# Kernel tuning notes

Hardware: AMD Instinct MI355X
Metric: run time of the kernel (lower is better)

## Reference

```python
import jax, jax.numpy as jnp
import numpy as np

N = 50000
E = 800000
D_IN, D_HID = 64, 128
EPS = 0.0


def setup_inputs() -> dict:
    key = jax.random.key(0)
    k1, k2, k3, k4 = jax.random.split(key, 4)
    x = jax.random.normal(k1, (N, D_IN), dtype=jnp.float32)
    edge_index = jax.random.randint(k2, (2, E), 0, N, dtype=jnp.int32)
    W1 = jax.random.normal(k3, (D_IN, D_HID), dtype=jnp.float32) * (1.0 / np.sqrt(D_IN))
    b1 = jnp.zeros((D_HID,), dtype=jnp.float32)
    W2 = jax.random.normal(k4, (D_HID, D_IN), dtype=jnp.float32) * (1.0 / np.sqrt(D_HID))
    b2 = jnp.zeros((D_IN,), dtype=jnp.float32)
    return {"x": x, "edge_index": edge_index, "W1": W1, "b1": b1, "W2": W2, "b2": b2}


def reference(x, edge_index, W1, b1, W2, b2):
    src = edge_index[0]
    dst = edge_index[1]
    # gather source node features [E, d] and scatter-add into destination nodes [N, d]
    agg = jax.ops.segment_sum(x[src], dst, num_segments=N)
    h = agg + (1.0 + EPS) * x
    # GIN MLP: Linear -> ReLU -> Linear
    h = jax.nn.relu(h @ W1 + b1)
    return h @ W2 + b2
```

## Files before the change

### kernel.cpp

```cpp
#include <hip/hip_runtime.h>

#define N_NODES 50000
#define N_EDGES 800000
#define D_INF 64
#define D_HIDF 128

#define NBUCKET ((N_NODES + 63) / 64)
#define CHUNK 4096
#define NCHUNK ((N_EDGES + CHUNK - 1) / CHUNK)
#define CAP 4096

typedef __attribute__((ext_vector_type(8))) short bf16x8v;
typedef __attribute__((ext_vector_type(4))) float f32x4;

__device__ __forceinline__ ushort f2bf(float f) {
    unsigned int u = __builtin_bit_cast(unsigned int, f);
    u += 0x7FFF + ((u >> 16) & 1);
    return (ushort)(u >> 16);
}
__device__ __forceinline__ float bf2f(ushort u) {
    return __builtin_bit_cast(float, ((unsigned int)u) << 16);
}
__device__ __forceinline__ float bflo(unsigned int w) {
    return __builtin_bit_cast(float, w << 16);
}
__device__ __forceinline__ float bfhi(unsigned int w) {
    return __builtin_bit_cast(float, w & 0xFFFF0000u);
}


#define CVT_N (N_NODES * D_INF / 8)
#define PREP_N (D_INF * D_HIDF)

__global__ void prep_kernel(const float* __restrict__ x, ushort* __restrict__ xb,
                            const float* __restrict__ W1, const float* __restrict__ W2,
                            ushort* __restrict__ w1tb, ushort* __restrict__ w2tb,
                            int* __restrict__ gcursor) {
    int gid = blockIdx.x * blockDim.x + threadIdx.x;
    if (gid < CVT_N) {
        float4 a = reinterpret_cast<const float4*>(x)[gid * 2];
        float4 b = reinterpret_cast<const float4*>(x)[gid * 2 + 1];
        ushort o[8] = {f2bf(a.x), f2bf(a.y), f2bf(a.z), f2bf(a.w),
                       f2bf(b.x), f2bf(b.y), f2bf(b.z), f2bf(b.w)};
        *reinterpret_cast<ulonglong2*>(xb + gid * 8) = *reinterpret_cast<ulonglong2*>(o);
    } else if (gid < CVT_N + PREP_N) {
        int i = gid - CVT_N;
        int j = i >> 6, l = i & 63;
        w1tb[i] = f2bf(W1[l * D_HIDF + j]);
        int d = i >> 7, jj = i & 127;
        w2tb[i] = f2bf(W2[jj * D_INF + d]);
    } else if (gid < CVT_N + PREP_N + NBUCKET) {
        int b = gid - CVT_N - PREP_N;
        gcursor[b] = b * CAP;
    } else if (gid < CVT_N + PREP_N + NBUCKET + 8) {
        int i = gid - CVT_N - PREP_N - NBUCKET;
        ulonglong2 z;
        z.x = 0; z.y = 0;
        *reinterpret_cast<ulonglong2*>(xb + (size_t)N_NODES * D_INF + i * 8) = z;
    }
}


__global__ void __launch_bounds__(512) sortfill_kernel(const int* __restrict__ src,
                                                       const int* __restrict__ dst,
                                                       int* __restrict__ gcursor,
                                                       unsigned int* __restrict__ binned) {
    __shared__ int cnt[NBUCKET];
    __shared__ int off[NBUCKET];
    __shared__ int cur[NBUCKET];
    __shared__ int gbase[NBUCKET];
    __shared__ unsigned int buf[CHUNK];
    __shared__ int wsum[8];

    int t = threadIdx.x;
    int lane = t & 63;
    int wv = t >> 6;
    int base = blockIdx.x * CHUNK;
    int chunk_n = min(CHUNK, N_EDGES - base);

    for (int i = t; i < NBUCKET; i += 512) cnt[i] = 0;
    __syncthreads();

    unsigned int pkr[8];
    int bkt[8];
#pragma unroll
    for (int k = 0; k < 8; k++) {
        int e = base + k * 512 + t;
        bkt[k] = -1;
        pkr[k] = 0;
        if (e < N_EDGES) {
            int d = dst[e];
            int s = src[e];
            pkr[k] = ((unsigned int)d << 16) | (unsigned int)s;
            bkt[k] = d >> 6;
            atomicAdd(&cnt[bkt[k]], 1);
        }
    }
    __syncthreads();

    {
        int b0 = t * 2;
        int v0 = (b0 < NBUCKET) ? cnt[b0] : 0;
        int v1 = (b0 + 1 < NBUCKET) ? cnt[b0 + 1] : 0;
        int s = v0 + v1;
        int incl = s;
#pragma unroll
        for (int o = 1; o < 64; o <<= 1) {
            int u = __shfl_up(incl, o);
            if (lane >= o) incl += u;
        }
        if (lane == 63) wsum[wv] = incl;
        __syncthreads();
        if (t == 0) {
#pragma unroll
            for (int w = 1; w < 8; w++) wsum[w] += wsum[w - 1];
        }
        __syncthreads();
        int run = ((wv > 0) ? wsum[wv - 1] : 0) + (incl - s);
        if (b0 < NBUCKET) {
            off[b0] = run;
            cur[b0] = run;
            if (v0 > 0) gbase[b0] = atomicAdd(&gcursor[b0], v0);
        }
        run += v0;
        if (b0 + 1 < NBUCKET) {
            off[b0 + 1] = run;
            cur[b0 + 1] = run;
            if (v1 > 0) gbase[b0 + 1] = atomicAdd(&gcursor[b0 + 1], v1);
        }
    }
    __syncthreads();

#pragma unroll
    for (int k = 0; k < 8; k++) {
        if (bkt[k] >= 0) {
            int r = atomicAdd(&cur[bkt[k]], 1);
            buf[r] = pkr[k];
        }
    }
    __syncthreads();

#pragma unroll
    for (int k = 0; k < CHUNK / 512; k++) {
        int slot = k * 512 + t;
        if (slot < chunk_n) {
            unsigned int pk = buf[slot];
            int b = pk >> 22;
            int idx = gbase[b] + (slot - off[b]);
            if (idx < (b + 1) * CAP) binned[idx] = pk;
        }
    }
}


#define AT_LD 72
#define HT_LD 136

__global__ void __launch_bounds__(1024) mega_kernel(
    const ushort* __restrict__ xb, const unsigned int* __restrict__ binned,
    const int* __restrict__ gcursor,
    const ushort* __restrict__ w1tb, const float* __restrict__ b1v,
    const ushort* __restrict__ w2tb, const float* __restrict__ b2v,
    float* __restrict__ out)
{
    __shared__ unsigned int seg[CAP];
    __shared__ unsigned int sorted[CAP + 16];
    __shared__ __align__(16) ushort atile[64 * AT_LD];
    __shared__ __align__(16) ushort htile[64 * HT_LD];
    __shared__ int c64[64];
    __shared__ int rb[65];
    __shared__ int o64[64];

    int t = threadIdx.x;
    int lane = t & 63;
    int wv = t >> 6;
    int b = blockIdx.x;
    int beg = b * CAP;
    int cnt = min(gcursor[b] - beg, CAP);
    int nb = b * 64;
    int nvalid = min(64, N_NODES - nb);

    if (t < 64) c64[t] = 0;
    __syncthreads();

    for (int i = t; i < cnt; i += 1024) {
        unsigned int pk = binned[beg + i];
        seg[i] = pk;
        atomicAdd(&c64[(pk >> 16) & 63], 1);
    }
    __syncthreads();
    if (t < 64) {
        int v = c64[t];
        int incl = v;
#pragma unroll
        for (int off = 1; off < 64; off <<= 1) {
            int u = __shfl_up(incl, off);
            if (t >= off) incl += u;
        }
        rb[t] = incl - v;
        o64[t] = incl - v;
        if (t == 63) rb[64] = incl;
    }
    __syncthreads();
    for (int i = t; i < cnt; i += 1024) {
        unsigned int pk = seg[i];
        int pos = atomicAdd(&o64[(pk >> 16) & 63], 1);
        sorted[pos] = pk;
    }
    __syncthreads();

    int g4 = lane >> 4;
    int f4 = lane & 15;
#pragma unroll
    for (int k = 0; k < 4; k++) {
        int n = wv * 4 + k;
        float a0 = 0.f, a1 = 0.f, a2 = 0.f, a3 = 0.f;
        if (n < nvalid) {
            int e = rb[n];
            int end = rb[n + 1];
#pragma unroll 2
            for (; e < end; e += 16) {
                int i0 = e + 0 + g4;
                int i1 = e + 4 + g4;
                int i2 = e + 8 + g4;
                int i3 = e + 12 + g4;
                unsigned int pk0 = (i0 < end) ? sorted[i0] : (unsigned int)N_NODES;
                unsigned int pk1 = (i1 < end) ? sorted[i1] : (unsigned int)N_NODES;
                unsigned int pk2 = (i2 < end) ? sorted[i2] : (unsigned int)N_NODES;
                unsigned int pk3 = (i3 < end) ? sorted[i3] : (unsigned int)N_NODES;
                uint2 v0 = *reinterpret_cast<const uint2*>(
                    &xb[(size_t)(pk0 & 0xFFFFu) * D_INF + f4 * 4]);
                uint2 v1 = *reinterpret_cast<const uint2*>(
                    &xb[(size_t)(pk1 & 0xFFFFu) * D_INF + f4 * 4]);
                uint2 v2 = *reinterpret_cast<const uint2*>(
                    &xb[(size_t)(pk2 & 0xFFFFu) * D_INF + f4 * 4]);
                uint2 v3 = *reinterpret_cast<const uint2*>(
                    &xb[(size_t)(pk3 & 0xFFFFu) * D_INF + f4 * 4]);
                a0 += bflo(v0.x); a1 += bfhi(v0.x); a2 += bflo(v0.y); a3 += bfhi(v0.y);
                a0 += bflo(v1.x); a1 += bfhi(v1.x); a2 += bflo(v1.y); a3 += bfhi(v1.y);
                a0 += bflo(v2.x); a1 += bfhi(v2.x); a2 += bflo(v2.y); a3 += bfhi(v2.y);
                a0 += bflo(v3.x); a1 += bfhi(v3.x); a2 += bflo(v3.y); a3 += bfhi(v3.y);
            }
            a0 += __shfl_xor(a0, 16); a0 += __shfl_xor(a0, 32);
            a1 += __shfl_xor(a1, 16); a1 += __shfl_xor(a1, 32);
            a2 += __shfl_xor(a2, 16); a2 += __shfl_xor(a2, 32);
            a3 += __shfl_xor(a3, 16); a3 += __shfl_xor(a3, 32);
        }
        if (g4 == 0 && n < 64) {
            if (n < nvalid) {
                uint2 v = *reinterpret_cast<const uint2*>(
                    &xb[(size_t)(nb + n) * D_INF + f4 * 4]);
                a0 += bflo(v.x); a1 += bfhi(v.x);
                a2 += bflo(v.y); a3 += bfhi(v.y);
            }
            unsigned int w0 = (unsigned int)f2bf(a0) | ((unsigned int)f2bf(a1) << 16);
            unsigned int w1 = (unsigned int)f2bf(a2) | ((unsigned int)f2bf(a3) << 16);
            *reinterpret_cast<uint2*>(&atile[n * AT_LD + f4 * 4]) = make_uint2(w0, w1);
        }
    }
    __syncthreads();

    int q = lane >> 4;
    int m = lane & 15;
    int mt = wv & 3;
    int arow = mt * 16 + m;
    int hrow0 = mt * 16 + q * 4;

    bf16x8v a0v = *reinterpret_cast<const bf16x8v*>(&atile[arow * AT_LD + q * 8]);
    bf16x8v a1v = *reinterpret_cast<const bf16x8v*>(&atile[arow * AT_LD + 32 + q * 8]);
    int jt0 = (wv >> 2) * 2;
#pragma unroll
    for (int jj = 0; jj < 2; jj++) {
        int j = (jt0 + jj) * 16 + m;
        bf16x8v bf0 = *reinterpret_cast<const bf16x8v*>(w1tb + j * D_INF + q * 8);
        bf16x8v bf1 = *reinterpret_cast<const bf16x8v*>(w1tb + j * D_INF + 32 + q * 8);
        f32x4 acc = {0.f, 0.f, 0.f, 0.f};
        acc = __builtin_amdgcn_mfma_f32_16x16x32_bf16(a0v, bf0, acc, 0, 0, 0);
        acc = __builtin_amdgcn_mfma_f32_16x16x32_bf16(a1v, bf1, acc, 0, 0, 0);
        float bv = b1v[j];
#pragma unroll
        for (int r = 0; r < 4; r++) {
            float hv = fmaxf(acc[r] + bv, 0.f);
            htile[(hrow0 + r) * HT_LD + j] = f2bf(hv);
        }
    }
    __syncthreads();

    bf16x8v ha0 = *reinterpret_cast<const bf16x8v*>(&htile[arow * HT_LD + 0 * 32 + q * 8]);
    bf16x8v ha1 = *reinterpret_cast<const bf16x8v*>(&htile[arow * HT_LD + 1 * 32 + q * 8]);
    bf16x8v ha2 = *reinterpret_cast<const bf16x8v*>(&htile[arow * HT_LD + 2 * 32 + q * 8]);
    bf16x8v ha3 = *reinterpret_cast<const bf16x8v*>(&htile[arow * HT_LD + 3 * 32 + q * 8]);
    {
        int d = (wv >> 2) * 16 + m;
        bf16x8v bw0 = *reinterpret_cast<const bf16x8v*>(w2tb + d * D_HIDF + 0 * 32 + q * 8);
        bf16x8v bw1 = *reinterpret_cast<const bf16x8v*>(w2tb + d * D_HIDF + 1 * 32 + q * 8);
        bf16x8v bw2 = *reinterpret_cast<const bf16x8v*>(w2tb + d * D_HIDF + 2 * 32 + q * 8);
        bf16x8v bw3 = *reinterpret_cast<const bf16x8v*>(w2tb + d * D_HIDF + 3 * 32 + q * 8);
        f32x4 acc = {0.f, 0.f, 0.f, 0.f};
        acc = __builtin_amdgcn_mfma_f32_16x16x32_bf16(ha0, bw0, acc, 0, 0, 0);
        acc = __builtin_amdgcn_mfma_f32_16x16x32_bf16(ha1, bw1, acc, 0, 0, 0);
        acc = __builtin_amdgcn_mfma_f32_16x16x32_bf16(ha2, bw2, acc, 0, 0, 0);
        acc = __builtin_amdgcn_mfma_f32_16x16x32_bf16(ha3, bw3, acc, 0, 0, 0);
        float bv = b2v[d];
#pragma unroll
        for (int r = 0; r < 4; r++) {
            int node = nb + hrow0 + r;
            if (node < N_NODES) out[(size_t)node * D_INF + d] = acc[r] + bv;
        }
    }
}


#define W1_LD 72
#define W2_LD 136

__global__ void __launch_bounds__(256) mlp_mfma_kernel(
    const ushort* __restrict__ aggb, const ushort* __restrict__ w1tb,
    const float* __restrict__ b1v, const ushort* __restrict__ w2tb,
    const float* __restrict__ b2v, float* __restrict__ out)
{
    __shared__ __align__(16) ushort atile[64 * AT_LD];
    __shared__ __align__(16) ushort w1s[128 * W1_LD];
    __shared__ __align__(16) ushort w2s[64 * W2_LD];
    __shared__ __align__(16) ushort htile[64 * HT_LD];

    int tid = threadIdx.x;
    int lane = tid & 63;
    int wv = tid >> 6;
    int nb = blockIdx.x * 64;

#pragma unroll
    for (int c = 0; c < 2; c++) {
        int chunk = tid + c * 256;
        int row = chunk >> 3;
        int col = (chunk & 7) * 8;
        ulonglong2 v;
        v.x = 0; v.y = 0;
        if (nb + row < N_NODES)
            v = *reinterpret_cast<const ulonglong2*>(aggb + (size_t)(nb + row) * D_INF + col);
        *reinterpret_cast<ulonglong2*>(&atile[row * AT_LD + col]) = v;
    }
#pragma unroll
    for (int c = 0; c < 4; c++) {
        int chunk = tid + c * 256;
        int row = chunk >> 3;
        int col = (chunk & 7) * 8;
        *reinterpret_cast<ulonglong2*>(&w1s[row * W1_LD + col]) =
            *reinterpret_cast<const ulonglong2*>(w1tb + row * 64 + col);
    }
#pragma unroll
    for (int c = 0; c < 4; c++) {
        int chunk = tid + c * 256;
        int row = chunk >> 4;
        int col = (chunk & 15) * 8;
        *reinterpret_cast<ulonglong2*>(&w2s[row * W2_LD + col]) =
            *reinterpret_cast<const ulonglong2*>(w2tb + row * 128 + col);
    }
    __syncthreads();

    int q = lane >> 4;
    int m = lane & 15;
    int arow = wv * 16 + m;
    int hrow0 = wv * 16 + q * 4;

    bf16x8v a0 = *reinterpret_cast<const bf16x8v*>(&atile[arow * AT_LD + q * 8]);
    bf16x8v a1 = *reinterpret_cast<const bf16x8v*>(&atile[arow * AT_LD + 32 + q * 8]);
#pragma unroll
    for (int jt = 0; jt < 8; jt++) {
        int j = jt * 16 + m;
        bf16x8v bf0 = *reinterpret_cast<const bf16x8v*>(&w1s[j * W1_LD + q * 8]);
        bf16x8v bf1 = *reinterpret_cast<const bf16x8v*>(&w1s[j * W1_LD + 32 + q * 8]);
        f32x4 acc = {0.f, 0.f, 0.f, 0.f};
        acc = __builtin_amdgcn_mfma_f32_16x16x32_bf16(a0, bf0, acc, 0, 0, 0);
        acc = __builtin_amdgcn_mfma_f32_16x16x32_bf16(a1, bf1, acc, 0, 0, 0);
        float bv = b1v[j];
#pragma unroll
        for (int r = 0; r < 4; r++) {
            float hv = fmaxf(acc[r] + bv, 0.f);
            htile[(hrow0 + r) * HT_LD + j] = f2bf(hv);
        }
    }

    bf16x8v ha0 = *reinterpret_cast<const bf16x8v*>(&htile[arow * HT_LD + 0 * 32 + q * 8]);
    bf16x8v ha1 = *reinterpret_cast<const bf16x8v*>(&htile[arow * HT_LD + 1 * 32 + q * 8]);
    bf16x8v ha2 = *reinterpret_cast<const bf16x8v*>(&htile[arow * HT_LD + 2 * 32 + q * 8]);
    bf16x8v ha3 = *reinterpret_cast<const bf16x8v*>(&htile[arow * HT_LD + 3 * 32 + q * 8]);
#pragma unroll
    for (int dt = 0; dt < 4; dt++) {
        int d = dt * 16 + m;
        f32x4 acc = {0.f, 0.f, 0.f, 0.f};
        bf16x8v bw0 = *reinterpret_cast<const bf16x8v*>(&w2s[d * W2_LD + 0 * 32 + q * 8]);
        bf16x8v bw1 = *reinterpret_cast<const bf16x8v*>(&w2s[d * W2_LD + 1 * 32 + q * 8]);
        bf16x8v bw2 = *reinterpret_cast<const bf16x8v*>(&w2s[d * W2_LD + 2 * 32 + q * 8]);
        bf16x8v bw3 = *reinterpret_cast<const bf16x8v*>(&w2s[d * W2_LD + 3 * 32 + q * 8]);
        acc = __builtin_amdgcn_mfma_f32_16x16x32_bf16(ha0, bw0, acc, 0, 0, 0);
        acc = __builtin_amdgcn_mfma_f32_16x16x32_bf16(ha1, bw1, acc, 0, 0, 0);
        acc = __builtin_amdgcn_mfma_f32_16x16x32_bf16(ha2, bw2, acc, 0, 0, 0);
        acc = __builtin_amdgcn_mfma_f32_16x16x32_bf16(ha3, bw3, acc, 0, 0, 0);
        float bv = b2v[d];
#pragma unroll
        for (int r = 0; r < 4; r++) {
            int node = nb + hrow0 + r;
            if (node < N_NODES) out[(size_t)node * D_INF + d] = acc[r] + bv;
        }
    }
}

__global__ void init_agg_kernel(const float* __restrict__ x, float* __restrict__ agg) {
    int i = blockIdx.x * blockDim.x + threadIdx.x;
    int n4 = N_NODES * D_INF / 4;
    if (i < n4) {
        reinterpret_cast<float4*>(agg)[i] = reinterpret_cast<const float4*>(x)[i];
    }
}

__global__ void scatter_kernel(const float* __restrict__ x,
                               const int* __restrict__ src,
                               const int* __restrict__ dst,
                               float* __restrict__ agg) {
    int tid = blockIdx.x * blockDim.x + threadIdx.x;
    int e = tid >> 6;
    int d = tid & 63;
    if (e < N_EDGES) {
        atomicAdd(&agg[(size_t)dst[e] * D_INF + d], x[(size_t)src[e] * D_INF + d]);
    }
}

__global__ void cvt_agg_kernel(const float* __restrict__ agg32, ushort* __restrict__ aggb) {
    int i = blockIdx.x * blockDim.x + threadIdx.x;
    if (i < N_NODES * D_INF) aggb[i] = f2bf(agg32[i]);
}

__global__ void prep_weights_only_kernel(const float* __restrict__ W1,
                                         const float* __restrict__ W2,
                                         ushort* __restrict__ w1tb,
                                         ushort* __restrict__ w2tb) {
    int i = blockIdx.x * blockDim.x + threadIdx.x;
    if (i < D_INF * D_HIDF) {
        int j = i >> 6, l = i & 63;
        w1tb[i] = f2bf(W1[l * D_HIDF + j]);
        int d = i >> 7, jj = i & 127;
        w2tb[i] = f2bf(W2[jj * D_INF + d]);
    }
}


extern "C" void kernel_launch(void* const* d_in, const int* in_sizes, int n_in,
                              void* d_out, int out_size, void* d_ws, size_t ws_size,
                              hipStream_t stream) {
    const float* x   = (const float*)d_in[0];
    const int* edge  = (const int*)d_in[1];
    const float* W1  = (const float*)d_in[2];
    const float* b1  = (const float*)d_in[3];
    const float* W2  = (const float*)d_in[4];
    const float* b2  = (const float*)d_in[5];
    float* out       = (float*)d_out;

    const int* src = edge;
    const int* dst = edge + N_EDGES;

    ushort* w1tb   = (ushort*)d_ws;
    ushort* w2tb   = w1tb + D_INF * D_HIDF;
    ushort* xb     = w2tb + D_INF * D_HIDF;
    int* gcursor   = (int*)(xb + (size_t)(N_NODES + 1) * D_INF);
    unsigned int* binned = (unsigned int*)(gcursor + NBUCKET);
    float* agg32   = (float*)xb;
    ushort* aggb   = (ushort*)(binned + (size_t)NBUCKET * CAP);

    size_t needed_full = (uintptr_t)(binned + (size_t)NBUCKET * CAP) - (uintptr_t)d_ws;
    size_t needed_fb   = (uintptr_t)(aggb + (size_t)N_NODES * D_INF) - (uintptr_t)d_ws;

    if (ws_size >= needed_full) {
        int prep_total = CVT_N + PREP_N + NBUCKET + 8;
        prep_kernel<<<(prep_total + 255) / 256, 256, 0, stream>>>(
            x, xb, W1, W2, w1tb, w2tb, gcursor);
        sortfill_kernel<<<NCHUNK, 512, 0, stream>>>(src, dst, gcursor, binned);
        mega_kernel<<<NBUCKET, 1024, 0, stream>>>(
            xb, binned, gcursor, w1tb, b1, w2tb, b2, out);
    } else if (ws_size >= needed_fb) {
        prep_weights_only_kernel<<<(PREP_N + 255) / 256, 256, 0, stream>>>(W1, W2, w1tb, w2tb);
        int n4 = N_NODES * D_INF / 4;
        init_agg_kernel<<<(n4 + 255) / 256, 256, 0, stream>>>(x, agg32);
        int work = N_EDGES * D_INF;
        scatter_kernel<<<(work + 255) / 256, 256, 0, stream>>>(x, src, dst, agg32);
        cvt_agg_kernel<<<(N_NODES * D_INF + 255) / 256, 256, 0, stream>>>(agg32, aggb);
        mlp_mfma_kernel<<<(N_NODES + 63) / 64, 256, 0, stream>>>(aggb, w1tb, b1, w2tb, b2, out);
    }
}
```

Measured before the change: 65.49 us.

## Fold x/weight bf16 conversion into the sortfill kernel as extra blocks

```diff
diff --git a/kernel.cpp b/kernel.cpp
--- a/kernel.cpp
+++ b/kernel.cpp
@@ -10,6 +10,11 @@
 #define NCHUNK ((N_EDGES + CHUNK - 1) / CHUNK)
 #define CAP 4096
 
+#define CVT_N (N_NODES * D_INF / 8)
+#define PREP_N (D_INF * D_HIDF)
+#define CVT_TOTAL (CVT_N + PREP_N + 8)
+#define CVT_BLKS ((CVT_TOTAL + 511) / 512)
+
 typedef __attribute__((ext_vector_type(8))) short bf16x8v;
 typedef __attribute__((ext_vector_type(4))) float f32x4;
 
@@ -29,42 +34,42 @@
 }
 
 
-#define CVT_N (N_NODES * D_INF / 8)
-#define PREP_N (D_INF * D_HIDF)
-
-__global__ void prep_kernel(const float* __restrict__ x, ushort* __restrict__ xb,
-                            const float* __restrict__ W1, const float* __restrict__ W2,
-                            ushort* __restrict__ w1tb, ushort* __restrict__ w2tb,
-                            int* __restrict__ gcursor) {
-    int gid = blockIdx.x * blockDim.x + threadIdx.x;
-    if (gid < CVT_N) {
-        float4 a = reinterpret_cast<const float4*>(x)[gid * 2];
-        float4 b = reinterpret_cast<const float4*>(x)[gid * 2 + 1];
-        ushort o[8] = {f2bf(a.x), f2bf(a.y), f2bf(a.z), f2bf(a.w),
-                       f2bf(b.x), f2bf(b.y), f2bf(b.z), f2bf(b.w)};
-        *reinterpret_cast<ulonglong2*>(xb + gid * 8) = *reinterpret_cast<ulonglong2*>(o);
-    } else if (gid < CVT_N + PREP_N) {
-        int i = gid - CVT_N;
-        int j = i >> 6, l = i & 63;
-        w1tb[i] = f2bf(W1[l * D_HIDF + j]);
-        int d = i >> 7, jj = i & 127;
-        w2tb[i] = f2bf(W2[jj * D_INF + d]);
-    } else if (gid < CVT_N + PREP_N + NBUCKET) {
-        int b = gid - CVT_N - PREP_N;
-        gcursor[b] = b * CAP;
-    } else if (gid < CVT_N + PREP_N + NBUCKET + 8) {
-        int i = gid - CVT_N - PREP_N - NBUCKET;
-        ulonglong2 z;
-        z.x = 0; z.y = 0;
-        *reinterpret_cast<ulonglong2*>(xb + (size_t)N_NODES * D_INF + i * 8) = z;
-    }
-}
-
-
-__global__ void __launch_bounds__(512) sortfill_kernel(const int* __restrict__ src,
-                                                       const int* __restrict__ dst,
-                                                       int* __restrict__ gcursor,
-                                                       unsigned int* __restrict__ binned) {
+__global__ void init_gcursor_kernel(int* __restrict__ gcursor) {
+    int i = blockIdx.x * blockDim.x + threadIdx.x;
+    if (i < NBUCKET) gcursor[i] = i * CAP;
+}
+
+
+__global__ void __launch_bounds__(512) sortfill_cvt_kernel(
+    const int* __restrict__ src, const int* __restrict__ dst,
+    int* __restrict__ gcursor, unsigned int* __restrict__ binned,
+    const float* __restrict__ x, ushort* __restrict__ xb,
+    const float* __restrict__ W1, const float* __restrict__ W2,
+    ushort* __restrict__ w1tb, ushort* __restrict__ w2tb)
+{
+    if (blockIdx.x >= NCHUNK) {
+        int gid = (blockIdx.x - NCHUNK) * 512 + threadIdx.x;
+        if (gid < CVT_N) {
+            float4 a = reinterpret_cast<const float4*>(x)[gid * 2];
+            float4 b = reinterpret_cast<const float4*>(x)[gid * 2 + 1];
+            ushort o[8] = {f2bf(a.x), f2bf(a.y), f2bf(a.z), f2bf(a.w),
+                           f2bf(b.x), f2bf(b.y), f2bf(b.z), f2bf(b.w)};
+            *reinterpret_cast<ulonglong2*>(xb + gid * 8) = *reinterpret_cast<ulonglong2*>(o);
+        } else if (gid < CVT_N + PREP_N) {
+            int i = gid - CVT_N;
+            int j = i >> 6, l = i & 63;
+            w1tb[i] = f2bf(W1[l * D_HIDF + j]);
+            int d = i >> 7, jj = i & 127;
+            w2tb[i] = f2bf(W2[jj * D_INF + d]);
+        } else if (gid < CVT_TOTAL) {
+            int i = gid - CVT_N - PREP_N;
+            ulonglong2 z;
+            z.x = 0; z.y = 0;
+            *reinterpret_cast<ulonglong2*>(xb + (size_t)N_NODES * D_INF + i * 8) = z;
+        }
+        return;
+    }
+
     __shared__ int cnt[NBUCKET];
     __shared__ int off[NBUCKET];
     __shared__ int cur[NBUCKET];
@@ -471,10 +476,9 @@
     size_t needed_fb   = (uintptr_t)(aggb + (size_t)N_NODES * D_INF) - (uintptr_t)d_ws;
 
     if (ws_size >= needed_full) {
-        int prep_total = CVT_N + PREP_N + NBUCKET + 8;
-        prep_kernel<<<(prep_total + 255) / 256, 256, 0, stream>>>(
-            x, xb, W1, W2, w1tb, w2tb, gcursor);
-        sortfill_kernel<<<NCHUNK, 512, 0, stream>>>(src, dst, gcursor, binned);
+        init_gcursor_kernel<<<(NBUCKET + 255) / 256, 256, 0, stream>>>(gcursor);
+        sortfill_cvt_kernel<<<NCHUNK + CVT_BLKS, 512, 0, stream>>>(
+            src, dst, gcursor, binned, x, xb, W1, W2, w1tb, w2tb);
         mega_kernel<<<NBUCKET, 1024, 0, stream>>>(
             xb, binned, gcursor, w1tb, b1, w2tb, b2, out);
     } else if (ws_size >= needed_fb) {
```

Result: no change. 64.30 us (-1.8%).
